# Kernel tuning notes

Hardware: AMD Instinct MI355X
Metric: run time of the kernel (lower is better)

## Reference

```python
import jax, jax.numpy as jnp
import numpy as np

B, C, H, W = 4, 64, 64, 64
CQK = C // 8


def setup_inputs() -> dict:
    key = jax.random.key(0)
    k0, k1, k2, k3, k4 = jax.random.split(key, 5)
    x = jax.random.normal(k0, (B, C, H, W), dtype=jnp.float32)
    # Conv1d kernel_size=1, bias=False -> plain [out, in] matmul weights
    Wq = jax.random.normal(k1, (CQK, C), dtype=jnp.float32) * 0.05
    Wk = jax.random.normal(k2, (CQK, C), dtype=jnp.float32) * 0.05
    Wv = jax.random.normal(k3, (C, C), dtype=jnp.float32) * 0.05
    # torch init is 0; use a nonzero scalar so the attention path is exercised
    gamma = jax.random.uniform(k4, (1,), dtype=jnp.float32)
    return {"x": x, "Wq": Wq, "Wk": Wk, "Wv": Wv, "gamma": gamma}


def reference(x, Wq, Wk, Wv, gamma):
    shape = x.shape                      # [B, C, H, W]
    xf = x.reshape(shape[0], shape[1], -1)  # [B, C, N]
    q = jnp.einsum('oc,bcn->bon', Wq, xf)   # [B, C/8, N]
    k = jnp.einsum('oc,bcn->bon', Wk, xf)   # [B, C/8, N]
    v = jnp.einsum('oc,bcn->bon', Wv, xf)   # [B, C, N]
    # score[b, n, m] = sum_c q[b, c, n] * k[b, c, m]  (no 1/sqrt(d) scale)
    score = jnp.einsum('bcn,bcm->bnm', q, k)  # [B, N, N]
    # unconventional softmax over dim=1 (rows/first N axis, i.e. per-column)
    score = jax.nn.softmax(score, axis=1)
    out = jnp.einsum('bcn,bnm->bcm', v, score)  # [B, C, N]
    attention = gamma * out + xf
    return attention.reshape(shape)
```

## Files before the change

### kernel.cpp

```cpp
#include <hip/hip_runtime.h>

#define BB 4
#define NN 4096

typedef __attribute__((ext_vector_type(8))) short short8v;
typedef __attribute__((ext_vector_type(4))) short short4v;
typedef __attribute__((ext_vector_type(4))) float float4v;

__device__ __forceinline__ unsigned short f2bf_rn(float f) {
    unsigned u = __float_as_uint(f);
    u += 0x7FFFu + ((u >> 16) & 1u);
    return (unsigned short)(u >> 16);
}

__global__ __launch_bounds__(256) void qkv_kernel(
    const float* __restrict__ x,
    const float* __restrict__ Wq, const float* __restrict__ Wk,
    const float* __restrict__ Wv,
    unsigned short* __restrict__ Qt, unsigned short* __restrict__ Kt,
    unsigned short* __restrict__ Vsw)
{
    __shared__ float xs[64][68];
    __shared__ float wl[64][81];
    __shared__ unsigned short Ot[80][72];

    const int t  = threadIdx.x;
    const int b  = blockIdx.y;
    const int n0 = blockIdx.x * 64;

    #pragma unroll
    for (int i = 0; i < 20; ++i) {
        int idx = t + 256 * i;
        int r = idx >> 6, c = idx & 63;
        float w;
        if (r < 8)       w = Wq[r * 64 + c];
        else if (r < 16) w = Wk[(r - 8) * 64 + c];
        else             w = Wv[(r - 16) * 64 + c];
        wl[c][r] = w;
    }
    #pragma unroll
    for (int i = 0; i < 4; ++i) {
        int idx = t + 256 * i;
        int c = idx >> 4, n4 = (idx & 15) * 4;
        *(float4*)&xs[c][n4] = *(const float4*)&x[(size_t)(b * 64 + c) * NN + n0 + n4];
    }
    __syncthreads();

    const int n4 = (t & 15) * 4;
    const int og = t >> 4;

    float acc[5][4];
    #pragma unroll
    for (int k = 0; k < 5; ++k)
        #pragma unroll
        for (int i = 0; i < 4; ++i) acc[k][i] = 0.f;

    for (int c = 0; c < 64; ++c) {
        float4 xv = *(const float4*)&xs[c][n4];
        #pragma unroll
        for (int k = 0; k < 5; ++k) {
            float wv = wl[c][og * 5 + k];
            acc[k][0] += wv * xv.x;
            acc[k][1] += wv * xv.y;
            acc[k][2] += wv * xv.z;
            acc[k][3] += wv * xv.w;
        }
    }

    #pragma unroll
    for (int k = 0; k < 5; ++k) {
        short4v pk;
        #pragma unroll
        for (int i = 0; i < 4; ++i) pk[i] = (short)f2bf_rn(acc[k][i]);
        *(short4v*)&Ot[og * 5 + k][n4] = pk;
    }
    __syncthreads();

    if (t < 128) {
        int n = t & 63;
        int rbase = (t < 64) ? 0 : 8;
        short8v p;
        #pragma unroll
        for (int j = 0; j < 8; ++j) p[j] = (short)Ot[rbase + j][n];
        unsigned short* dst = ((t < 64) ? Qt : Kt) + ((size_t)b * NN + n0 + n) * 8;
        *(short8v*)dst = p;
    }

    {
        int ci = t >> 5, s = t & 31;
        int ct = ci >> 1, nbl = ci & 1;
        size_t nb = (size_t)blockIdx.x * 2 + nbl;
        unsigned short* cb = Vsw + ((size_t)(b * 4 + ct) * 128 + nb) * 512;
        #pragma unroll
        for (int h = 0; h < 2; ++h) {
            int l = s * 2 + h;
            short8v d = *(short8v*)&Ot[16 + ct * 16 + (l & 15)][nbl * 32 + ((l >> 4) << 3)];
            *(short8v*)(cb + l * 8) = d;
        }
    }
}

__global__ __launch_bounds__(256, 4) void attn_kernel(
    const unsigned short* __restrict__ Qt,
    const unsigned short* __restrict__ Kt,
    const unsigned short* __restrict__ Vsw,
    const float* __restrict__ x, const float* __restrict__ gamma,
    float* __restrict__ out)
{
    __shared__ __align__(16) unsigned short Pb[4][2][16][40];
    __shared__ float Ored[4][64][17];
    __shared__ float Lred[4][16];
    __shared__ float Lf[16];

    const int t    = threadIdx.x;
    const int w    = t >> 6;
    const int lane = t & 63;
    const int quad = lane >> 4;
    const int l15  = lane & 15;
    const int b    = blockIdx.y;
    const int m0   = blockIdx.x * 16;

    const short8v zfrag = {0, 0, 0, 0, 0, 0, 0, 0};
    const float4v zacc  = {0.f, 0.f, 0.f, 0.f};

    short8v bk = zfrag;
    if (quad == 0)
        bk = *(const short8v*)(Kt + (size_t)(b * NN + m0 + l15) * 8);

    float4v acc[4];
    #pragma unroll
    for (int ct = 0; ct < 4; ++ct) acc[ct] = zacc;
    float Lacc = 0.f;

    const unsigned short* qrow = Qt + (size_t)(b * NN + w * 1024 + l15) * 8;
    const unsigned short* vptr = Vsw + ((size_t)b * 4 * 128 + w * 32) * 512 + lane * 8;

    short8v av0 = *(const short8v*)(vptr);
    short8v av1 = *(const short8v*)(vptr + 1 * 128 * 512);
    short8v av2 = *(const short8v*)(vptr + 2 * 128 * 512);
    short8v av3 = *(const short8v*)(vptr + 3 * 128 * 512);
    {
        short8v aq0 = zfrag, aq1 = zfrag;
        if (quad == 0) {
            aq0 = *(const short8v*)(qrow);
            aq1 = *(const short8v*)(qrow + 16 * 8);
        }
        float4v s0 = __builtin_amdgcn_mfma_f32_16x16x32_bf16(aq0, bk, zacc, 0, 0, 0);
        float4v s1 = __builtin_amdgcn_mfma_f32_16x16x32_bf16(aq1, bk, zacc, 0, 0, 0);
        float p[8];
        #pragma unroll
        for (int j = 0; j < 4; ++j) p[j]     = __expf(s0[j]);
        #pragma unroll
        for (int j = 0; j < 4; ++j) p[4 + j] = __expf(s1[j]);
        #pragma unroll
        for (int j = 0; j < 8; ++j) Lacc += p[j];
        short4v pk0, pk1;
        #pragma unroll
        for (int j = 0; j < 4; ++j) {
            pk0[j] = (short)f2bf_rn(p[j]);
            pk1[j] = (short)f2bf_rn(p[4 + j]);
        }
        *(short4v*)&Pb[w][0][l15][quad * 4]      = pk0;
        *(short4v*)&Pb[w][0][l15][16 + quad * 4] = pk1;
    }

    for (int it = 0; it < 31; ++it) {
        const int itn = it + 1;

        short8v avn0 = *(const short8v*)(vptr + itn * 512);
        short8v avn1 = *(const short8v*)(vptr + 1 * 128 * 512 + itn * 512);
        short8v avn2 = *(const short8v*)(vptr + 2 * 128 * 512 + itn * 512);
        short8v avn3 = *(const short8v*)(vptr + 3 * 128 * 512 + itn * 512);

        short8v aq0 = zfrag, aq1 = zfrag;
        if (quad == 0) {
            aq0 = *(const short8v*)(qrow + (size_t)(itn * 32) * 8);
            aq1 = *(const short8v*)(qrow + (size_t)(itn * 32 + 16) * 8);
        }
        float4v s0 = __builtin_amdgcn_mfma_f32_16x16x32_bf16(aq0, bk, zacc, 0, 0, 0);
        float4v s1 = __builtin_amdgcn_mfma_f32_16x16x32_bf16(aq1, bk, zacc, 0, 0, 0);
        float p[8];
        #pragma unroll
        for (int j = 0; j < 4; ++j) p[j]     = __expf(s0[j]);
        #pragma unroll
        for (int j = 0; j < 4; ++j) p[4 + j] = __expf(s1[j]);
        #pragma unroll
        for (int j = 0; j < 8; ++j) Lacc += p[j];
        short4v pk0, pk1;
        #pragma unroll
        for (int j = 0; j < 4; ++j) {
            pk0[j] = (short)f2bf_rn(p[j]);
            pk1[j] = (short)f2bf_rn(p[4 + j]);
        }
        *(short4v*)&Pb[w][itn & 1][l15][quad * 4]      = pk0;
        *(short4v*)&Pb[w][itn & 1][l15][16 + quad * 4] = pk1;

        short8v bp = *(const short8v*)&Pb[w][it & 1][l15][quad * 8];
        acc[0] = __builtin_amdgcn_mfma_f32_16x16x32_bf16(av0, bp, acc[0], 0, 0, 0);
        acc[1] = __builtin_amdgcn_mfma_f32_16x16x32_bf16(av1, bp, acc[1], 0, 0, 0);
        acc[2] = __builtin_amdgcn_mfma_f32_16x16x32_bf16(av2, bp, acc[2], 0, 0, 0);
        acc[3] = __builtin_amdgcn_mfma_f32_16x16x32_bf16(av3, bp, acc[3], 0, 0, 0);

        av0 = avn0; av1 = avn1; av2 = avn2; av3 = avn3;
    }

    {
        short8v bp = *(const short8v*)&Pb[w][1][l15][quad * 8];
        acc[0] = __builtin_amdgcn_mfma_f32_16x16x32_bf16(av0, bp, acc[0], 0, 0, 0);
        acc[1] = __builtin_amdgcn_mfma_f32_16x16x32_bf16(av1, bp, acc[1], 0, 0, 0);
        acc[2] = __builtin_amdgcn_mfma_f32_16x16x32_bf16(av2, bp, acc[2], 0, 0, 0);
        acc[3] = __builtin_amdgcn_mfma_f32_16x16x32_bf16(av3, bp, acc[3], 0, 0, 0);
    }

    Lacc += __shfl_xor(Lacc, 16, 64);
    Lacc += __shfl_xor(Lacc, 32, 64);
    if (lane < 16) Lred[w][lane] = Lacc;

    #pragma unroll
    for (int ct = 0; ct < 4; ++ct)
        #pragma unroll
        for (int r = 0; r < 4; ++r)
            Ored[w][ct * 16 + quad * 4 + r][l15] = acc[ct][r];
    __syncthreads();

    if (t < 16)
        Lf[t] = 1.f / (Lred[0][t] + Lred[1][t] + Lred[2][t] + Lred[3][t]);
    __syncthreads();

    {
        const float gv = gamma[0];
        int c = t >> 2, m4 = (t & 3) * 4;
        float4 o;
        #pragma unroll
        for (int i = 0; i < 4; ++i) {
            float s = Ored[0][c][m4 + i] + Ored[1][c][m4 + i]
                    + Ored[2][c][m4 + i] + Ored[3][c][m4 + i];
            ((float*)&o)[i] = s * Lf[m4 + i];
        }
        size_t gbase = (size_t)(b * 64 + c) * NN + m0 + m4;
        float4 xv = *(const float4*)&x[gbase];
        float4 r;
        r.x = gv * o.x + xv.x; r.y = gv * o.y + xv.y;
        r.z = gv * o.z + xv.z; r.w = gv * o.w + xv.w;
        *(float4*)&out[gbase] = r;
    }
}

extern "C" void kernel_launch(void* const* d_in, const int* in_sizes, int n_in,
                              void* d_out, int out_size, void* d_ws, size_t ws_size,
                              hipStream_t stream) {
    const float* x     = (const float*)d_in[0];
    const float* Wq    = (const float*)d_in[1];
    const float* Wk    = (const float*)d_in[2];
    const float* Wv    = (const float*)d_in[3];
    const float* gamma = (const float*)d_in[4];
    float* out = (float*)d_out;

    unsigned short* ws = (unsigned short*)d_ws;
    unsigned short* Qt  = ws;
    unsigned short* Kt  = Qt + (size_t)BB * NN * 8;
    unsigned short* Vsw = Kt + (size_t)BB * NN * 8;

    qkv_kernel<<<dim3(NN / 64, BB), 256, 0, stream>>>(x, Wq, Wk, Wv, Qt, Kt, Vsw);
    attn_kernel<<<dim3(NN / 16, BB), 256, 0, stream>>>(Qt, Kt, Vsw, x, gamma, out);
}
```

Before: 97.10 us.

## Widen attention tile to 64 columns with shared-memory staged V and Q

The attention kernel now handles 64 output columns per block instead of 16. Its four waves are split two by two over column halves and key halves, and each V and Q tile is staged cooperatively in double-buffered shared memory, so one global V load feeds two waves. This cuts redundant global V reads by a factor of four across blocks. The cost is a block-wide barrier every iteration, fewer blocks (256 instead of 1024), and more LDS. The qkv kernel is re-tiled to 32 columns per block to match the new V swizzle layout.

```diff
diff --git a/kernel.cpp b/kernel.cpp
--- a/kernel.cpp
+++ b/kernel.cpp
@@ -20,13 +20,14 @@
     unsigned short* __restrict__ Qt, unsigned short* __restrict__ Kt,
     unsigned short* __restrict__ Vsw)
 {
-    __shared__ float xs[64][68];
+    __shared__ float xs[64][36];
     __shared__ float wl[64][81];
-    __shared__ unsigned short Ot[80][72];
+    __shared__ unsigned short Ot[80][40];
 
     const int t  = threadIdx.x;
     const int b  = blockIdx.y;
-    const int n0 = blockIdx.x * 64;
+    const int nb = blockIdx.x;
+    const int n0 = nb * 32;
 
     #pragma unroll
     for (int i = 0; i < 20; ++i) {
@@ -39,210 +40,221 @@
         wl[c][r] = w;
     }
     #pragma unroll
-    for (int i = 0; i < 4; ++i) {
+    for (int i = 0; i < 2; ++i) {
         int idx = t + 256 * i;
-        int c = idx >> 4, n4 = (idx & 15) * 4;
+        int c = idx >> 3, n4 = (idx & 7) * 4;
         *(float4*)&xs[c][n4] = *(const float4*)&x[(size_t)(b * 64 + c) * NN + n0 + n4];
     }
     __syncthreads();
 
-    const int n4 = (t & 15) * 4;
+    const int n2 = (t & 15) * 2;
     const int og = t >> 4;
 
-    float acc[5][4];
-    #pragma unroll
-    for (int k = 0; k < 5; ++k)
-        #pragma unroll
-        for (int i = 0; i < 4; ++i) acc[k][i] = 0.f;
+    float acc[5][2];
+    #pragma unroll
+    for (int k = 0; k < 5; ++k) { acc[k][0] = 0.f; acc[k][1] = 0.f; }
 
     for (int c = 0; c < 64; ++c) {
-        float4 xv = *(const float4*)&xs[c][n4];
+        float2 xv = *(const float2*)&xs[c][n2];
         #pragma unroll
         for (int k = 0; k < 5; ++k) {
             float wv = wl[c][og * 5 + k];
             acc[k][0] += wv * xv.x;
             acc[k][1] += wv * xv.y;
-            acc[k][2] += wv * xv.z;
-            acc[k][3] += wv * xv.w;
         }
     }
 
     #pragma unroll
     for (int k = 0; k < 5; ++k) {
-        short4v pk;
-        #pragma unroll
-        for (int i = 0; i < 4; ++i) pk[i] = (short)f2bf_rn(acc[k][i]);
-        *(short4v*)&Ot[og * 5 + k][n4] = pk;
-    }
-    __syncthreads();
-
-    if (t < 128) {
-        int n = t & 63;
-        int rbase = (t < 64) ? 0 : 8;
+        Ot[og * 5 + k][n2]     = f2bf_rn(acc[k][0]);
+        Ot[og * 5 + k][n2 + 1] = f2bf_rn(acc[k][1]);
+    }
+    __syncthreads();
+
+    if (t < 64) {
+        int n = t & 31;
+        int rbase = (t < 32) ? 0 : 8;
         short8v p;
         #pragma unroll
         for (int j = 0; j < 8; ++j) p[j] = (short)Ot[rbase + j][n];
-        unsigned short* dst = ((t < 64) ? Qt : Kt) + ((size_t)b * NN + n0 + n) * 8;
+        unsigned short* dst = ((t < 32) ? Qt : Kt) + ((size_t)b * NN + n0 + n) * 8;
         *(short8v*)dst = p;
     }
 
     {
-        int ci = t >> 5, s = t & 31;
-        int ct = ci >> 1, nbl = ci & 1;
-        size_t nb = (size_t)blockIdx.x * 2 + nbl;
+        int ct = t >> 6, l = t & 63;
         unsigned short* cb = Vsw + ((size_t)(b * 4 + ct) * 128 + nb) * 512;
-        #pragma unroll
-        for (int h = 0; h < 2; ++h) {
-            int l = s * 2 + h;
-            short8v d = *(short8v*)&Ot[16 + ct * 16 + (l & 15)][nbl * 32 + ((l >> 4) << 3)];
-            *(short8v*)(cb + l * 8) = d;
-        }
-    }
-}
-
-__global__ __launch_bounds__(256, 4) void attn_kernel(
+        short8v d = *(short8v*)&Ot[16 + ct * 16 + (l & 15)][(l >> 4) * 8];
+        *(short8v*)(cb + l * 8) = d;
+    }
+}
+
+__global__ __launch_bounds__(256) void attn_kernel(
     const unsigned short* __restrict__ Qt,
     const unsigned short* __restrict__ Kt,
     const unsigned short* __restrict__ Vsw,
     const float* __restrict__ x, const float* __restrict__ gamma,
     float* __restrict__ out)
 {
-    __shared__ __align__(16) unsigned short Pb[4][2][16][40];
-    __shared__ float Ored[4][64][17];
-    __shared__ float Lred[4][16];
-    __shared__ float Lf[16];
+    __shared__ __align__(16) unsigned short Vs[2][2][2048];
+    __shared__ __align__(16) unsigned short Qs[2][2][256];
+    __shared__ __align__(16) unsigned short Pb[4][2][32][40];
+    __shared__ float Ored[2][2][64][33];
+    __shared__ float Lred[4][2][16];
+    __shared__ float Lf[64];
 
     const int t    = threadIdx.x;
     const int w    = t >> 6;
     const int lane = t & 63;
     const int quad = lane >> 4;
     const int l15  = lane & 15;
+    const int mh   = w & 1;
+    const int nh   = w >> 1;
     const int b    = blockIdx.y;
-    const int m0   = blockIdx.x * 16;
+    const int m0   = blockIdx.x * 64;
 
     const short8v zfrag = {0, 0, 0, 0, 0, 0, 0, 0};
     const float4v zacc  = {0.f, 0.f, 0.f, 0.f};
 
-    short8v bk = zfrag;
-    if (quad == 0)
-        bk = *(const short8v*)(Kt + (size_t)(b * NN + m0 + l15) * 8);
-
-    float4v acc[4];
-    #pragma unroll
-    for (int ct = 0; ct < 4; ++ct) acc[ct] = zacc;
-    float Lacc = 0.f;
-
-    const unsigned short* qrow = Qt + (size_t)(b * NN + w * 1024 + l15) * 8;
-    const unsigned short* vptr = Vsw + ((size_t)b * 4 * 128 + w * 32) * 512 + lane * 8;
-
-    short8v av0 = *(const short8v*)(vptr);
-    short8v av1 = *(const short8v*)(vptr + 1 * 128 * 512);
-    short8v av2 = *(const short8v*)(vptr + 2 * 128 * 512);
-    short8v av3 = *(const short8v*)(vptr + 3 * 128 * 512);
+    short8v bk0 = zfrag, bk1 = zfrag;
+    if (quad == 0) {
+        bk0 = *(const short8v*)(Kt + (size_t)(b * NN + m0 + mh * 32 + l15) * 8);
+        bk1 = *(const short8v*)(Kt + (size_t)(b * NN + m0 + mh * 32 + 16 + l15) * 8);
+    }
+
+    float4v acc[4][2];
+    #pragma unroll
+    for (int ct = 0; ct < 4; ++ct) { acc[ct][0] = zacc; acc[ct][1] = zacc; }
+    float Lacc0 = 0.f, Lacc1 = 0.f;
+
+    const int sct = t >> 6, ss = t & 63;
+    const unsigned short* vsrc0 = Vsw + ((size_t)(b * 4 + sct) * 128 + 0)  * 512 + ss * 8;
+    const unsigned short* vsrc1 = Vsw + ((size_t)(b * 4 + sct) * 128 + 64) * 512 + ss * 8;
+    const int qnh = t >> 5, qrw = t & 31;
+    const unsigned short* qsrc = Qt + ((size_t)b * NN + qnh * 64 * 32 + qrw) * 8;
+
     {
-        short8v aq0 = zfrag, aq1 = zfrag;
-        if (quad == 0) {
-            aq0 = *(const short8v*)(qrow);
-            aq1 = *(const short8v*)(qrow + 16 * 8);
-        }
-        float4v s0 = __builtin_amdgcn_mfma_f32_16x16x32_bf16(aq0, bk, zacc, 0, 0, 0);
-        float4v s1 = __builtin_amdgcn_mfma_f32_16x16x32_bf16(aq1, bk, zacc, 0, 0, 0);
-        float p[8];
-        #pragma unroll
-        for (int j = 0; j < 4; ++j) p[j]     = __expf(s0[j]);
-        #pragma unroll
-        for (int j = 0; j < 4; ++j) p[4 + j] = __expf(s1[j]);
-        #pragma unroll
-        for (int j = 0; j < 8; ++j) Lacc += p[j];
-        short4v pk0, pk1;
-        #pragma unroll
-        for (int j = 0; j < 4; ++j) {
-            pk0[j] = (short)f2bf_rn(p[j]);
-            pk1[j] = (short)f2bf_rn(p[4 + j]);
-        }
-        *(short4v*)&Pb[w][0][l15][quad * 4]      = pk0;
-        *(short4v*)&Pb[w][0][l15][16 + quad * 4] = pk1;
-    }
-
-    for (int it = 0; it < 31; ++it) {
-        const int itn = it + 1;
-
-        short8v avn0 = *(const short8v*)(vptr + itn * 512);
-        short8v avn1 = *(const short8v*)(vptr + 1 * 128 * 512 + itn * 512);
-        short8v avn2 = *(const short8v*)(vptr + 2 * 128 * 512 + itn * 512);
-        short8v avn3 = *(const short8v*)(vptr + 3 * 128 * 512 + itn * 512);
-
-        short8v aq0 = zfrag, aq1 = zfrag;
-        if (quad == 0) {
-            aq0 = *(const short8v*)(qrow + (size_t)(itn * 32) * 8);
-            aq1 = *(const short8v*)(qrow + (size_t)(itn * 32 + 16) * 8);
-        }
-        float4v s0 = __builtin_amdgcn_mfma_f32_16x16x32_bf16(aq0, bk, zacc, 0, 0, 0);
-        float4v s1 = __builtin_amdgcn_mfma_f32_16x16x32_bf16(aq1, bk, zacc, 0, 0, 0);
-        float p[8];
-        #pragma unroll
-        for (int j = 0; j < 4; ++j) p[j]     = __expf(s0[j]);
-        #pragma unroll
-        for (int j = 0; j < 4; ++j) p[4 + j] = __expf(s1[j]);
-        #pragma unroll
-        for (int j = 0; j < 8; ++j) Lacc += p[j];
-        short4v pk0, pk1;
-        #pragma unroll
-        for (int j = 0; j < 4; ++j) {
-            pk0[j] = (short)f2bf_rn(p[j]);
-            pk1[j] = (short)f2bf_rn(p[4 + j]);
-        }
-        *(short4v*)&Pb[w][itn & 1][l15][quad * 4]      = pk0;
-        *(short4v*)&Pb[w][itn & 1][l15][16 + quad * 4] = pk1;
-
-        short8v bp = *(const short8v*)&Pb[w][it & 1][l15][quad * 8];
-        acc[0] = __builtin_amdgcn_mfma_f32_16x16x32_bf16(av0, bp, acc[0], 0, 0, 0);
-        acc[1] = __builtin_amdgcn_mfma_f32_16x16x32_bf16(av1, bp, acc[1], 0, 0, 0);
-        acc[2] = __builtin_amdgcn_mfma_f32_16x16x32_bf16(av2, bp, acc[2], 0, 0, 0);
-        acc[3] = __builtin_amdgcn_mfma_f32_16x16x32_bf16(av3, bp, acc[3], 0, 0, 0);
-
-        av0 = avn0; av1 = avn1; av2 = avn2; av3 = avn3;
-    }
-
-    {
-        short8v bp = *(const short8v*)&Pb[w][1][l15][quad * 8];
-        acc[0] = __builtin_amdgcn_mfma_f32_16x16x32_bf16(av0, bp, acc[0], 0, 0, 0);
-        acc[1] = __builtin_amdgcn_mfma_f32_16x16x32_bf16(av1, bp, acc[1], 0, 0, 0);
-        acc[2] = __builtin_amdgcn_mfma_f32_16x16x32_bf16(av2, bp, acc[2], 0, 0, 0);
-        acc[3] = __builtin_amdgcn_mfma_f32_16x16x32_bf16(av3, bp, acc[3], 0, 0, 0);
-    }
-
-    Lacc += __shfl_xor(Lacc, 16, 64);
-    Lacc += __shfl_xor(Lacc, 32, 64);
-    if (lane < 16) Lred[w][lane] = Lacc;
+        *(short8v*)&Vs[0][0][sct * 512 + ss * 8] = *(const short8v*)(vsrc0);
+        *(short8v*)&Vs[0][1][sct * 512 + ss * 8] = *(const short8v*)(vsrc1);
+        if (t < 64)
+            *(short8v*)&Qs[0][qnh][qrw * 8] = *(const short8v*)(qsrc);
+    }
+
+    for (int i = 0; i <= 64; ++i) {
+        short8v vreg0, vreg1, qreg;
+        if (i <= 62) {
+            vreg0 = *(const short8v*)(vsrc0 + (size_t)(i + 1) * 512);
+            vreg1 = *(const short8v*)(vsrc1 + (size_t)(i + 1) * 512);
+            if (t < 64) qreg = *(const short8v*)(qsrc + (size_t)(i + 1) * 32 * 8);
+        }
+
+        short8v av0, av1, av2, av3, bp0, bp1;
+        if (i >= 1) {
+            const int rb = (i - 1) & 1;
+            av0 = *(const short8v*)&Vs[rb][nh][0 * 512 + lane * 8];
+            av1 = *(const short8v*)&Vs[rb][nh][1 * 512 + lane * 8];
+            av2 = *(const short8v*)&Vs[rb][nh][2 * 512 + lane * 8];
+            av3 = *(const short8v*)&Vs[rb][nh][3 * 512 + lane * 8];
+            bp0 = *(const short8v*)&Pb[w][rb][l15][quad * 8];
+            bp1 = *(const short8v*)&Pb[w][rb][16 + l15][quad * 8];
+        }
+        __syncthreads();
+
+        if (i <= 63) {
+            if (i <= 62) {
+                const int wb = (i + 1) & 1;
+                *(short8v*)&Vs[wb][0][sct * 512 + ss * 8] = vreg0;
+                *(short8v*)&Vs[wb][1][sct * 512 + ss * 8] = vreg1;
+                if (t < 64) *(short8v*)&Qs[wb][qnh][qrw * 8] = qreg;
+            }
+
+            const int cb = i & 1;
+            short8v aq0 = zfrag, aq1 = zfrag;
+            if (quad == 0) {
+                aq0 = *(const short8v*)&Qs[cb][nh][l15 * 8];
+                aq1 = *(const short8v*)&Qs[cb][nh][(16 + l15) * 8];
+            }
+            float4v s00 = __builtin_amdgcn_mfma_f32_16x16x32_bf16(aq0, bk0, zacc, 0, 0, 0);
+            float4v s01 = __builtin_amdgcn_mfma_f32_16x16x32_bf16(aq0, bk1, zacc, 0, 0, 0);
+            float4v s10 = __builtin_amdgcn_mfma_f32_16x16x32_bf16(aq1, bk0, zacc, 0, 0, 0);
+            float4v s11 = __builtin_amdgcn_mfma_f32_16x16x32_bf16(aq1, bk1, zacc, 0, 0, 0);
+
+            float p00[4], p01[4], p10[4], p11[4];
+            #pragma unroll
+            for (int j = 0; j < 4; ++j) {
+                p00[j] = __expf(s00[j]); p01[j] = __expf(s01[j]);
+                p10[j] = __expf(s10[j]); p11[j] = __expf(s11[j]);
+            }
+            #pragma unroll
+            for (int j = 0; j < 4; ++j) {
+                Lacc0 += p00[j] + p10[j];
+                Lacc1 += p01[j] + p11[j];
+            }
+            short4v k00, k01, k10, k11;
+            #pragma unroll
+            for (int j = 0; j < 4; ++j) {
+                k00[j] = (short)f2bf_rn(p00[j]); k01[j] = (short)f2bf_rn(p01[j]);
+                k10[j] = (short)f2bf_rn(p10[j]); k11[j] = (short)f2bf_rn(p11[j]);
+            }
+            *(short4v*)&Pb[w][cb][l15][quad * 4]           = k00;
+            *(short4v*)&Pb[w][cb][l15][16 + quad * 4]      = k10;
+            *(short4v*)&Pb[w][cb][16 + l15][quad * 4]      = k01;
+            *(short4v*)&Pb[w][cb][16 + l15][16 + quad * 4] = k11;
+        }
+
+        if (i >= 1) {
+            acc[0][0] = __builtin_amdgcn_mfma_f32_16x16x32_bf16(av0, bp0, acc[0][0], 0, 0, 0);
+            acc[1][0] = __builtin_amdgcn_mfma_f32_16x16x32_bf16(av1, bp0, acc[1][0], 0, 0, 0);
+            acc[2][0] = __builtin_amdgcn_mfma_f32_16x16x32_bf16(av2, bp0, acc[2][0], 0, 0, 0);
+            acc[3][0] = __builtin_amdgcn_mfma_f32_16x16x32_bf16(av3, bp0, acc[3][0], 0, 0, 0);
+            acc[0][1] = __builtin_amdgcn_mfma_f32_16x16x32_bf16(av0, bp1, acc[0][1], 0, 0, 0);
+            acc[1][1] = __builtin_amdgcn_mfma_f32_16x16x32_bf16(av1, bp1, acc[1][1], 0, 0, 0);
+            acc[2][1] = __builtin_amdgcn_mfma_f32_16x16x32_bf16(av2, bp1, acc[2][1], 0, 0, 0);
+            acc[3][1] = __builtin_amdgcn_mfma_f32_16x16x32_bf16(av3, bp1, acc[3][1], 0, 0, 0);
+        }
+    }
+
+    Lacc0 += __shfl_xor(Lacc0, 16, 64);
+    Lacc0 += __shfl_xor(Lacc0, 32, 64);
+    Lacc1 += __shfl_xor(Lacc1, 16, 64);
+    Lacc1 += __shfl_xor(Lacc1, 32, 64);
+    if (lane < 16) {
+        Lred[w][0][lane] = Lacc0;
+        Lred[w][1][lane] = Lacc1;
+    }
 
     #pragma unroll
     for (int ct = 0; ct < 4; ++ct)
         #pragma unroll
-        for (int r = 0; r < 4; ++r)
-            Ored[w][ct * 16 + quad * 4 + r][l15] = acc[ct][r];
-    __syncthreads();
-
-    if (t < 16)
-        Lf[t] = 1.f / (Lred[0][t] + Lred[1][t] + Lred[2][t] + Lred[3][t]);
+        for (int msub = 0; msub < 2; ++msub)
+            #pragma unroll
+            for (int r = 0; r < 4; ++r)
+                Ored[nh][mh][ct * 16 + quad * 4 + r][msub * 16 + l15] = acc[ct][msub][r];
+    __syncthreads();
+
+    if (t < 64) {
+        int mh_t = t >> 5, msub_t = (t >> 4) & 1, l_t = t & 15;
+        Lf[t] = 1.f / (Lred[mh_t][msub_t][l_t] + Lred[2 + mh_t][msub_t][l_t]);
+    }
     __syncthreads();
 
     {
         const float gv = gamma[0];
-        int c = t >> 2, m4 = (t & 3) * 4;
-        float4 o;
-        #pragma unroll
-        for (int i = 0; i < 4; ++i) {
-            float s = Ored[0][c][m4 + i] + Ored[1][c][m4 + i]
-                    + Ored[2][c][m4 + i] + Ored[3][c][m4 + i];
-            ((float*)&o)[i] = s * Lf[m4 + i];
-        }
-        size_t gbase = (size_t)(b * 64 + c) * NN + m0 + m4;
-        float4 xv = *(const float4*)&x[gbase];
-        float4 r;
-        r.x = gv * o.x + xv.x; r.y = gv * o.y + xv.y;
-        r.z = gv * o.z + xv.z; r.w = gv * o.w + xv.w;
-        *(float4*)&out[gbase] = r;
+        int c = t >> 2, q = t & 3;
+        #pragma unroll
+        for (int i4 = 0; i4 < 4; ++i4) {
+            int ml64 = q * 16 + i4 * 4;
+            int mhh = ml64 >> 5, ml32 = ml64 & 31;
+            size_t gbase = (size_t)(b * 64 + c) * NN + m0 + ml64;
+            float4 xv = *(const float4*)&x[gbase];
+            float4 r;
+            #pragma unroll
+            for (int e = 0; e < 4; ++e) {
+                float o = Ored[0][mhh][c][ml32 + e] + Ored[1][mhh][c][ml32 + e];
+                ((float*)&r)[e] = gv * o * Lf[ml64 + e] + ((float*)&xv)[e];
+            }
+            *(float4*)&out[gbase] = r;
+        }
     }
 }
 
@@ -261,6 +273,6 @@
     unsigned short* Kt  = Qt + (size_t)BB * NN * 8;
     unsigned short* Vsw = Kt + (size_t)BB * NN * 8;
 
-    qkv_kernel<<<dim3(NN / 64, BB), 256, 0, stream>>>(x, Wq, Wk, Wv, Qt, Kt, Vsw);
-    attn_kernel<<<dim3(NN / 16, BB), 256, 0, stream>>>(Qt, Kt, Vsw, x, gamma, out);
-}
+    qkv_kernel<<<dim3(NN / 32, BB), 256, 0, stream>>>(x, Wq, Wk, Wv, Qt, Kt, Vsw);
+    attn_kernel<<<dim3(NN / 64, BB), 256, 0, stream>>>(Qt, Kt, Vsw, x, gamma, out);
+}
```

After: 115.6 us. +19.0%, slower.
